# Kernel optimization log

Measured on AMD Instinct MI355X. Metric: run time of the kernel, lower is better.

## Reference

```python
import jax, jax.numpy as jnp
import numpy as np

DS = 16                      # downsample
DEPTH_MIN, DEPTH_MAX = 1.0, 60.0
XB = (-51.2, 51.2, 0.4)      # bev_x_bound
YB = (-51.2, 51.2, 0.4)      # bev_y_bound
ZB = (-5.0, 3.0)             # bev_z_bound (min, max)
BEV_H = int((YB[1] - YB[0]) / YB[2])   # 256
BEV_W = int((XB[1] - XB[0]) / XB[2])   # 256


def setup_inputs() -> dict:
    key = jax.random.key(0)
    k1, k2 = jax.random.split(key)
    B, N, C, H, W, D = 2, 6, 128, 16, 44, 64
    feat = jax.random.normal(k1, (B, N, C, H, W), dtype=jnp.float32)
    # depth distribution: softmax over depth bins (as a real LSS depth head produces)
    depth = jax.nn.softmax(jax.random.normal(k2, (B, N, D, H, W), dtype=jnp.float32), axis=2)
    # intrinsics chosen so that after the module's internal K scaling the frustum
    # rays actually spread over the BEV grid (non-degenerate valid mask)
    K = np.array([[2.0, 0.0, 1.34], [0.0, 2.0, 0.47], [0.0, 0.0, 1.0]], dtype=np.float32)
    intrinsics = np.broadcast_to(K, (B, N, 3, 3)).copy()
    # 6 cameras looking outward: cam(x right, y down, z fwd) -> ego(x fwd, y left, z up), yawed
    base = np.array([[0, 0, 1], [-1, 0, 0], [0, -1, 0]], dtype=np.float32)
    Es = []
    for yaw in np.linspace(0.0, 2.0 * np.pi, N, endpoint=False):
        c, s = np.cos(yaw), np.sin(yaw)
        Rz = np.array([[c, -s, 0], [s, c, 0], [0, 0, 1]], dtype=np.float32)
        E = np.eye(4, dtype=np.float32)
        E[:3, :3] = Rz @ base
        E[:3, 3] = [1.0 * c, 1.0 * s, 1.5]
        Es.append(E)
    extrinsics = np.broadcast_to(np.stack(Es), (B, N, 4, 4)).copy()
    return {
        "feat": feat,
        "depth": depth,
        "intrinsics": jnp.asarray(intrinsics),
        "extrinsics": jnp.asarray(extrinsics),
        "img_h": 256,
        "img_w": 704,
    }


def _forward(feat, depth, intrinsics, extrinsics, img_h, img_w):
    B, N, C, H, W = feat.shape
    D = depth.shape[2]
    dt = feat.dtype
    # frustum (D,H,W) of pixel coords u,v and metric depth d
    dbins = jnp.linspace(DEPTH_MIN, DEPTH_MAX, D).astype(dt)
    yy, xx = jnp.meshgrid(jnp.arange(H, dtype=dt), jnp.arange(W, dtype=dt), indexing='ij')
    u = jnp.broadcast_to(xx[None], (D, H, W)).reshape(-1)
    v = jnp.broadcast_to(yy[None], (D, H, W)).reshape(-1)
    d = jnp.broadcast_to(dbins[:, None, None], (D, H, W)).reshape(-1)
    # intrinsics scaled exactly as the torch module does (rows 0,1 scaled)
    scale_x = W / (img_w / DS)
    scale_y = H / (img_h / DS)
    rs = jnp.array([DS / scale_x, DS / scale_y, 1.0], dtype=dt)
    K = intrinsics * rs[:, None]            # (B,N,3,3)
    Kinv = jnp.linalg.inv(K)
    uvd = jnp.stack([u * d, v * d, d], axis=-1)     # (P,3), P = D*H*W
    pc = jnp.einsum('bnij,pj->bnpi', Kinv, uvd)     # camera-frame points
    R = extrinsics[..., :3, :3]
    t = extrinsics[..., :3, 3]
    pts = jnp.einsum('bnij,bnpj->bnpi', R, pc) + t[:, :, None, :]   # (B,N,P,3) ego
    pts = pts.reshape(B, -1, 3)                     # (B, N*P, 3)
    # depth-lift: feat (B,N,C,H,W) x depth (B,N,D,H,W) -> (B, N*D*H*W, C)
    lifted = (feat[:, :, :, None] * depth[:, :, None]).transpose(0, 1, 3, 4, 5, 2).reshape(B, -1, C)
    # voxelize (torch .long() truncates toward zero; so does astype here)
    xi = ((pts[..., 0] - XB[0]) / XB[2]).astype(jnp.int32)
    yi = ((pts[..., 1] - YB[0]) / YB[2]).astype(jnp.int32)
    valid = (xi >= 0) & (xi < BEV_W) & (yi >= 0) & (yi < BEV_H) & \
            (pts[..., 2] >= ZB[0]) & (pts[..., 2] <= ZB[1])
    idx = jnp.where(valid, yi * BEV_W + xi, 0)      # invalid -> cell 0 with zeroed value
    vals = lifted * valid[..., None].astype(dt)
    seg = lambda val, i: jax.ops.segment_sum(val, i, num_segments=BEV_H * BEV_W)
    bev = jax.vmap(seg)(vals, idx)                  # (B, cells, C)
    cnt = jax.vmap(seg)(valid.astype(dt), idx)      # (B, cells)
    bev = bev.transpose(0, 2, 1).reshape(B, C, BEV_H, BEV_W)
    cnt = cnt.reshape(B, 1, BEV_H, BEV_W)
    return bev / (cnt + 1e-5)


def reference(feat, depth, intrinsics, extrinsics, img_h, img_w):
    return _forward(feat, depth, intrinsics, extrinsics, img_h, img_w)
```

## Files before the change

kernel.cpp:

```cpp
#include <hip/hip_runtime.h>
#include <hip/hip_bf16.h>

#define Bc 2
#define Nc 6
#define Cc 128
#define Hc 16
#define Wc 44
#define Dc 64
#define HWc (Hc*Wc)
#define BNc (Bc*Nc)
#define NRAY (Nc*HWc)
#define NPTS (Bc*Nc*Dc*HWc)
#define BEV_W 256
#define BEV_H 256
#define BEV_HW (BEV_W*BEV_H)
#define NSEG (Bc*BEV_HW)
#define GT 16
#define NTILE (NSEG/GT)
#define NSCANB 512
#define GNB 1056
#define GNW (GNB*4)

#define OFF_KI    0
#define OFF_DB    512
#define OFF_CNT   1024
#define OFF_OFFS  (OFF_CNT  + 524288)
#define OFF_FILL  (OFF_OFFS + 524288)
#define OFF_BSUM  (OFF_FILL + 524288)
#define OFF_E8    (OFF_BSUM + 4096)
#define OFF_FT    (OFF_E8   + 4325376)
#define WS_NEED   (OFF_FT   + 4325376)
#define OFF_ACC   (OFF_FT   + 4325376)
#define WS_BIG    (OFF_ACC  + 67108864)
#define OFF_FIDX  OFF_E8
#define OFF_FCNT  OFF_CNT

__device__ __forceinline__ void setup_into(int tid, const float* __restrict__ intr,
                                           const int* __restrict__ p_imgh,
                                           const int* __restrict__ p_imgw,
                                           float* Ki, float* db) {
    if (tid < Dc) {
        double v = 1.0 + (double)tid * (59.0 / 63.0);
        db[tid] = (tid == Dc - 1) ? 60.0f : (float)v;
    }
    if (tid >= BNc) return;
    double img_h = (double)p_imgh[0];
    double img_w = (double)p_imgw[0];
    double scale_x = (double)Wc / (img_w / 16.0);
    double scale_y = (double)Hc / (img_h / 16.0);
    float rs0 = (float)(16.0 / scale_x);
    float rs1 = (float)(16.0 / scale_y);
    float rs2 = 1.0f;
    const float* K = intr + tid * 9;
    float k0 = __fmul_rn(K[0], rs0), k1 = __fmul_rn(K[1], rs0), k2 = __fmul_rn(K[2], rs0);
    float k3 = __fmul_rn(K[3], rs1), k4 = __fmul_rn(K[4], rs1), k5 = __fmul_rn(K[5], rs1);
    float k6 = __fmul_rn(K[6], rs2), k7 = __fmul_rn(K[7], rs2), k8 = __fmul_rn(K[8], rs2);
    float c0 = __fsub_rn(__fmul_rn(k4,k8), __fmul_rn(k5,k7));
    float c1 = __fsub_rn(__fmul_rn(k3,k8), __fmul_rn(k5,k6));
    float c2 = __fsub_rn(__fmul_rn(k3,k7), __fmul_rn(k4,k6));
    float det = __fadd_rn(__fsub_rn(__fmul_rn(k0,c0), __fmul_rn(k1,c1)), __fmul_rn(k2,c2));
    float* o = Ki + tid * 9;
    o[0] = __fdiv_rn(c0, det);
    o[1] = __fdiv_rn(__fsub_rn(__fmul_rn(k2,k7), __fmul_rn(k1,k8)), det);
    o[2] = __fdiv_rn(__fsub_rn(__fmul_rn(k1,k5), __fmul_rn(k2,k4)), det);
    o[3] = __fdiv_rn(__fsub_rn(__fmul_rn(k5,k6), __fmul_rn(k3,k8)), det);
    o[4] = __fdiv_rn(__fsub_rn(__fmul_rn(k0,k8), __fmul_rn(k2,k6)), det);
    o[5] = __fdiv_rn(__fsub_rn(__fmul_rn(k2,k3), __fmul_rn(k0,k5)), det);
    o[6] = __fdiv_rn(c2, det);
    o[7] = __fdiv_rn(__fsub_rn(__fmul_rn(k1,k6), __fmul_rn(k0,k7)), det);
    o[8] = __fdiv_rn(__fsub_rn(__fmul_rn(k0,k4), __fmul_rn(k1,k3)), det);
}

__global__ void k_setup(const float* __restrict__ intr, const float* __restrict__ extr,
                        const int* __restrict__ p_imgh, const int* __restrict__ p_imgw,
                        float* __restrict__ Ki, float* __restrict__ db) {
    setup_into(threadIdx.x, intr, p_imgh, p_imgw, Ki, db);
}

__device__ __forceinline__ int classify_point(int gid, const float* Ki_all,
                                              const float* db, const float* extr) {
    int p   = gid % HWc;
    int tmp = gid / HWc;
    int d   = tmp % Dc;
    int bn  = tmp / Dc;
    int w = p % Wc, h = p / Wc;
    float dd = db[d];
    float ud = __fmul_rn((float)w, dd);
    float vd = __fmul_rn((float)h, dd);
    const float* Ki = Ki_all + bn * 9;
    float pcx = fmaf(Ki[2], dd, fmaf(Ki[1], vd, __fmul_rn(Ki[0], ud)));
    float pcy = fmaf(Ki[5], dd, fmaf(Ki[4], vd, __fmul_rn(Ki[3], ud)));
    float pcz = fmaf(Ki[8], dd, fmaf(Ki[7], vd, __fmul_rn(Ki[6], ud)));
    const float* E = extr + bn * 16;
    float px = __fadd_rn(fmaf(E[2],  pcz, fmaf(E[1], pcy, __fmul_rn(E[0], pcx))), E[3]);
    float py = __fadd_rn(fmaf(E[6],  pcz, fmaf(E[5], pcy, __fmul_rn(E[4], pcx))), E[7]);
    float pz = __fadd_rn(fmaf(E[10], pcz, fmaf(E[9], pcy, __fmul_rn(E[8], pcx))), E[11]);
    float fx = __fdiv_rn(__fsub_rn(px, -51.2f), 0.4f);
    float fy = __fdiv_rn(__fsub_rn(py, -51.2f), 0.4f);
    int xi = (int)fx;
    int yi = (int)fy;
    bool valid = (xi >= 0) && (xi < BEV_W) && (yi >= 0) && (yi < BEV_H)
              && (pz >= -5.0f) && (pz <= 3.0f);
    return valid ? (yi * BEV_W + xi) : -1;
}

__device__ __forceinline__ void scan_bsum(int tid, const int* __restrict__ bsum,
                                          int* sB, int* su, int* pEtotS) {
    int2 v2 = ((const int2*)bsum)[tid];
    int s = v2.x + v2.y;
    su[tid] = s;
    __syncthreads();
    for (int st = 1; st < 256; st <<= 1) {
        int t2 = (tid >= st) ? su[tid - st] : 0;
        __syncthreads();
        su[tid] += t2;
        __syncthreads();
    }
    int base = su[tid] - s;
    sB[2 * tid]     = base;
    sB[2 * tid + 1] = base + v2.x;
    if (tid == 255) *pEtotS = base + s;
    __syncthreads();
}

__device__ __forceinline__ unsigned long long lanemask_le(int lane) {
    return (lane == 63) ? ~0ull : ((1ull << (lane + 1)) - 1ull);
}

__global__ __launch_bounds__(256) void k_count(const float* __restrict__ intr,
                                               const float* __restrict__ extr,
                                               const int* __restrict__ p_imgh,
                                               const int* __restrict__ p_imgw,
                                               const float* __restrict__ feat,
                                               int* __restrict__ cntArr,
                                               float* __restrict__ ft) {
    __shared__ float sKi[BNc * 9];
    __shared__ float sDb[Dc];
    __shared__ float buf[Cc * 17];
    int tid = threadIdx.x;
    setup_into(tid, intr, p_imgh, p_imgw, sKi, sDb);
    __syncthreads();
    int gid = blockIdx.x * 256 + tid;
    int cell = classify_point(gid, sKi, sDb, extr);
    {
        int lane = tid & 63;
        int b = gid / (Nc * Dc * HWc);
        int seg = b * BEV_HW + cell;
        int key = (cell >= 0) ? seg : -1;
        int pk  = __shfl_up(key, 1);
        bool bnd = (lane == 0) || (key != pk);
        unsigned long long bm = __ballot(bnd);
        if (key >= 0 && bnd) {
            unsigned long long rest = (lane == 63) ? 0ull : (bm >> (lane + 1));
            int runlen = (rest != 0ull) ? __ffsll((long long)rest) : (64 - lane);
            atomicAdd(&cntArr[seg], runlen);
        }
    }
    if (blockIdx.x < BNc * (HWc / 16)) {
        int bn   = blockIdx.x / (HWc / 16);
        int tile = blockIdx.x % (HWc / 16);
        const float* fb = feat + (size_t)bn * Cc * HWc + tile * 16;
        for (int i = tid; i < Cc * 16; i += 256) {
            int c = i >> 4, hw = i & 15;
            buf[c * 17 + hw] = fb[c * HWc + hw];
        }
        __syncthreads();
        float* obt = ft + ((size_t)bn * HWc + tile * 16) * Cc;
        for (int i = tid; i < 16 * Cc; i += 256) {
            int r = i >> 7, ch = i & 127;
            obt[(size_t)r * Cc + ch] = buf[ch * 17 + r];
        }
    }
}

__global__ __launch_bounds__(256) void k_scanB(const int* __restrict__ cntArr,
                                               int* __restrict__ offs,
                                               int* __restrict__ fill,
                                               int* __restrict__ bsum) {
    __shared__ int su[256];
    int tid = threadIdx.x;
    int g = blockIdx.x * 256 + tid;
    int v = cntArr[g];
    su[tid] = v;
    __syncthreads();
    for (int st = 1; st < 256; st <<= 1) {
        int t2 = (tid >= st) ? su[tid - st] : 0;
        __syncthreads();
        su[tid] += t2;
        __syncthreads();
    }
    int e = su[tid] - v;
    offs[g] = e;
    fill[g] = e;
    if (tid == 255) bsum[blockIdx.x] = su[255];
}

__global__ __launch_bounds__(256) void k_fill(const float* __restrict__ intr,
                                              const float* __restrict__ extr,
                                              const int* __restrict__ p_imgh,
                                              const int* __restrict__ p_imgw,
                                              const float* __restrict__ depth,
                                              int* __restrict__ fill,
                                              const int* __restrict__ bsum,
                                              int2* __restrict__ e8) {
    __shared__ float sKi[BNc * 9];
    __shared__ float sDb[Dc];
    __shared__ int   sB[NSCANB];
    __shared__ int   su[256];
    __shared__ int   sEtot;
    int tid = threadIdx.x;
    setup_into(tid, intr, p_imgh, p_imgw, sKi, sDb);
    scan_bsum(tid, bsum, sB, su, &sEtot);
    int gid = blockIdx.x * 256 + tid;
    int cell = classify_point(gid, sKi, sDb, extr);
    int lane = tid & 63;
    int bnum = gid / (Nc * Dc * HWc);
    int seg = bnum * BEV_HW + cell;
    int key = (cell >= 0) ? seg : -1;
    int pk  = __shfl_up(key, 1);
    bool bnd = (lane == 0) || (key != pk);
    unsigned long long bm = __ballot(bnd);
    int base = 0;
    if (key >= 0 && bnd) {
        unsigned long long rest = (lane == 63) ? 0ull : (bm >> (lane + 1));
        int runlen = (rest != 0ull) ? __ffsll((long long)rest) : (64 - lane);
        base = atomicAdd(&fill[seg], runlen) + sB[seg >> 8];
    }
    int headLane = 63 - __clzll(bm & lanemask_le(lane));
    int myBase = __shfl(base, headLane);
    if (key >= 0) {
        int p   = gid % HWc;
        int bn  = gid / (Dc * HWc);
        int ray = (bn % Nc) * HWc + p;
        e8[myBase + (lane - headLane)] = make_int2(ray | (seg << 13),
                                                   __float_as_int(depth[gid]));
    }
}

__global__ __launch_bounds__(256) void k_gather2(const float2* __restrict__ ft2,
                                                 const int2* __restrict__ e8,
                                                 const int* __restrict__ cntArr,
                                                 const int* __restrict__ offs,
                                                 const int* __restrict__ bsum,
                                                 float* __restrict__ acc) {
    __shared__ int sB[NSCANB];
    __shared__ int su[256];
    __shared__ int sEtot;
    int tid = threadIdx.x;
    scan_bsum(tid, bsum, sB, su, &sEtot);
    int Etot = sEtot;
    int wid  = blockIdx.x * 4 + (tid >> 6);
    int lane = tid & 63;
    int WCH  = (Etot + GNW - 1) / GNW;
    if (WCH <= 0) return;
    int start = wid * WCH;
    if (start >= Etot) return;
    int end = start + WCH; if (end > Etot) end = Etot;
    int k0 = 0;
    if (start > 0) {
        int segP = e8[start - 1].x >> 13;
        k0 = offs[segP] + sB[segP >> 8] + cntArr[segP];
        if (k0 >= end) return;
    }
    int segE = e8[end - 1].x >> 13;
    int kend = offs[segE] + sB[segE >> 8] + cntArr[segE];
    int total = kend - k0;

    float2 a = make_float2(0.f, 0.f);
    int curc = -1;
    const int U = 8;
    int nb = total / U;
    if (nb > 0) {
        int2 e[U];
        #pragma unroll
        for (int u = 0; u < U; u++) e[u] = e8[k0 + u];
        for (int g = 0; g < nb; g++) {
            float2 f[U];
            #pragma unroll
            for (int u = 0; u < U; u++) {
                int sx = e[u].x;
                f[u] = ft2[((size_t)((sx >> 29) * NRAY) + (sx & 8191)) * 64 + lane];
            }
            int2 en[U];
            if (g + 1 < nb) {
                #pragma unroll
                for (int u = 0; u < U; u++) en[u] = e8[k0 + (g + 1) * U + u];
            } else {
                #pragma unroll
                for (int u = 0; u < U; u++) en[u] = e[u];
            }
            #pragma unroll
            for (int u = 0; u < U; u++) {
                int sg = e[u].x >> 13;
                if (sg != curc) {
                    if (curc >= 0) *(float2*)(acc + (size_t)curc * Cc + 2 * lane) = a;
                    curc = sg; a.x = 0.f; a.y = 0.f;
                }
                float ww = __int_as_float(e[u].y);
                a.x = fmaf(ww, f[u].x, a.x);
                a.y = fmaf(ww, f[u].y, a.y);
            }
            #pragma unroll
            for (int u = 0; u < U; u++) e[u] = en[u];
        }
    }
    for (int j = nb * U; j < total; j++) {
        int2 ee = e8[k0 + j];
        int sg = ee.x >> 13;
        if (sg != curc) {
            if (curc >= 0) *(float2*)(acc + (size_t)curc * Cc + 2 * lane) = a;
            curc = sg; a.x = 0.f; a.y = 0.f;
        }
        float ww = __int_as_float(ee.y);
        float2 f = ft2[((size_t)((ee.x >> 29) * NRAY) + (ee.x & 8191)) * 64 + lane];
        a.x = fmaf(ww, f.x, a.x);
        a.y = fmaf(ww, f.y, a.y);
    }
    if (curc >= 0) *(float2*)(acc + (size_t)curc * Cc + 2 * lane) = a;
}

__global__ __launch_bounds__(256) void k_finish(const float* __restrict__ acc,
                                                const int* __restrict__ cntArr,
                                                float* __restrict__ out) {
    __shared__ float res[GT * 132];
    __shared__ float sInv[GT];
    __shared__ int   sC[GT + 1];
    int seg0  = blockIdx.x * GT;
    int b     = seg0 >> 16;
    int cell0 = seg0 & 65535;
    int tid = threadIdx.x;
    if (tid < 64) {
        int n = (tid < GT) ? cntArr[seg0 + tid] : 0;
        int v = n;
        #pragma unroll
        for (int d = 1; d < GT; d <<= 1) {
            int y = __shfl_up(v, d, GT);
            if ((tid & (GT - 1)) >= d) v += y;
        }
        if (tid < GT) {
            sC[tid] = n;
            sInv[tid] = __fdiv_rn(1.0f, __fadd_rn((float)n, 1e-5f));
            if (tid == GT - 1) sC[GT] = v;
        }
    }
    __syncthreads();
    float* ob = out + (size_t)b * Cc * BEV_HW + cell0;
    if (sC[GT] == 0) {
        float4 z = {0.f, 0.f, 0.f, 0.f};
        for (int i = tid; i < Cc * GT / 4; i += 256) {
            int q = i & 3, c = i >> 2;
            *(float4*)(ob + (size_t)c * BEV_HW + q * 4) = z;
        }
        return;
    }
    {
        int g0 = tid >> 5, l32 = tid & 31;
        #pragma unroll
        for (int pass = 0; pass < 2; pass++) {
            int g = g0 + pass * 8;
            float4 v;
            if (sC[g] > 0) v = *(const float4*)(acc + (size_t)(seg0 + g) * Cc + 4 * l32);
            else           v = make_float4(0.f, 0.f, 0.f, 0.f);
            *(float4*)(&res[g * 132 + 4 * l32]) = v;
        }
    }
    __syncthreads();
    for (int i = tid; i < Cc * GT / 4; i += 256) {
        int q = i & 3, c = i >> 2;
        float4 v;
        #pragma unroll
        for (int kk = 0; kk < 4; kk++) {
            int g = q * 4 + kk;
            (&v.x)[kk] = __fmul_rn(res[g * 132 + c], sInv[g]);
        }
        *(float4*)(ob + (size_t)c * BEV_HW + q * 4) = v;
    }
}

__global__ __launch_bounds__(256) void k_classifyF(const float* __restrict__ Ki_all,
                                                   const float* __restrict__ db,
                                                   const float* __restrict__ extr,
                                                   int* __restrict__ idxT,
                                                   float* __restrict__ cnt) {
    int gid = blockIdx.x * 256 + threadIdx.x;
    if (gid >= NPTS) return;
    int cell = classify_point(gid, Ki_all, db, extr);
    idxT[gid] = cell;
    if (cell >= 0) {
        int b = gid / (Nc * Dc * HWc);
        atomicAdd(&cnt[b * BEV_HW + cell], 1.0f);
    }
}

__global__ __launch_bounds__(256) void k_scatterF(const float* __restrict__ feat,
                                                  const float* __restrict__ depth,
                                                  const int* __restrict__ idxT,
                                                  float* __restrict__ out) {
    __shared__ float s_dw[HWc];
    __shared__ int   s_idx[HWc];
    int blk = blockIdx.x;
    int bn  = blk / Dc;
    int b   = bn / Nc;
    int tid = threadIdx.x;
    const float* dp = depth + (size_t)blk * HWc;
    const int*   ip = idxT  + (size_t)blk * HWc;
    for (int p = tid; p < HWc; p += 256) { s_dw[p] = dp[p]; s_idx[p] = ip[p]; }
    __syncthreads();
    const float* fb = feat + (size_t)bn * Cc * HWc;
    float*       ob = out  + (size_t)b  * Cc * BEV_HW;
    for (int c = 0; c < Cc; c++) {
        const float* f = fb + (size_t)c * HWc;
        float*       o = ob + (size_t)c * BEV_HW;
        for (int p = tid; p < HWc; p += 256) {
            int cell = s_idx[p];
            if (cell >= 0) atomicAdd(&o[cell], __fmul_rn(f[p], s_dw[p]));
        }
    }
}

__global__ __launch_bounds__(256) void k_normF(float* __restrict__ out,
                                               const float* __restrict__ cnt) {
    int i = blockIdx.x * 256 + threadIdx.x;
    const int total = Bc * Cc * BEV_HW / 4;
    if (i >= total) return;
    int q = i % (BEV_HW / 4);
    int b = i / (Cc * BEV_HW / 4);
    float4 v = ((float4*)out)[i];
    float4 cv = ((const float4*)cnt)[b * (BEV_HW / 4) + q];
    v.x = __fdiv_rn(v.x, __fadd_rn(cv.x, 1e-5f));
    v.y = __fdiv_rn(v.y, __fadd_rn(cv.y, 1e-5f));
    v.z = __fdiv_rn(v.z, __fadd_rn(cv.z, 1e-5f));
    v.w = __fdiv_rn(v.w, __fadd_rn(cv.w, 1e-5f));
    ((float4*)out)[i] = v;
}

extern "C" void kernel_launch(void* const* d_in, const int* in_sizes, int n_in,
                              void* d_out, int out_size, void* d_ws, size_t ws_size,
                              hipStream_t stream) {
    const float* feat  = (const float*)d_in[0];
    const float* depth = (const float*)d_in[1];
    const float* intr  = (const float*)d_in[2];
    const float* extr  = (const float*)d_in[3];
    const int*   imh   = (const int*)d_in[4];
    const int*   imw   = (const int*)d_in[5];
    float* out = (float*)d_out;
    char*  ws  = (char*)d_ws;

    if (ws_size >= (size_t)WS_BIG) {
        int*   cntA = (int*)(ws + OFF_CNT);
        int*   offs = (int*)(ws + OFF_OFFS);
        int*   fill = (int*)(ws + OFF_FILL);
        int*   bsum = (int*)(ws + OFF_BSUM);
        int2*  e8   = (int2*)(ws + OFF_E8);
        float* ft   = (float*)(ws + OFF_FT);
        float* acc  = (float*)(ws + OFF_ACC);

        hipMemsetAsync(cntA, 0, (size_t)NSEG * sizeof(int), stream);
        k_count<<<NPTS / 256, 256, 0, stream>>>(intr, extr, imh, imw, feat, cntA, ft);
        k_scanB<<<NSCANB, 256, 0, stream>>>(cntA, offs, fill, bsum);
        k_fill<<<NPTS / 256, 256, 0, stream>>>(intr, extr, imh, imw, depth, fill, bsum, e8);
        k_gather2<<<GNB, 256, 0, stream>>>((const float2*)ft, e8, cntA, offs, bsum, acc);
        k_finish<<<NTILE, 256, 0, stream>>>(acc, cntA, out);
    } else {
        float* Ki   = (float*)(ws + OFF_KI);
        float* db   = (float*)(ws + OFF_DB);
        int*   idxT = (int*)(ws + OFF_FIDX);
        float* cnt  = (float*)(ws + OFF_FCNT);
        hipMemsetAsync(out, 0, (size_t)out_size * sizeof(float), stream);
        hipMemsetAsync(cnt, 0, (size_t)Bc * BEV_HW * sizeof(float), stream);
        k_setup<<<1, 64, 0, stream>>>(intr, extr, imh, imw, Ki, db);
        k_classifyF<<<(NPTS + 255) / 256, 256, 0, stream>>>(Ki, db, extr, idxT, cnt);
        k_scatterF<<<Bc * Nc * Dc, 256, 0, stream>>>(feat, depth, idxT, out);
        k_normF<<<(Bc * Cc * BEV_HW / 4 + 255) / 256, 256, 0, stream>>>(out, cnt);
    }
}
```

Before: 152.1 us.

## Fuse normalization into gather, precompute ranks in count pass, drop finish kernel

The count kernel now records each point's segment and its rank within that segment. The fill kernel then becomes a simple scatter, with no second classification and no atomics, using a fully scanned offsets array produced by a new small scan kernel. The gather kernel stages per-warp accumulators for 16-cell groups in shared memory and writes normalized output directly. Extra blocks zero the empty cells. This removes the 64MB accumulator round trip and the finish kernel. In exchange, output writes are strided and less coalesced, and there is an extra pk buffer pass.

```diff
diff --git a/kernel.cpp b/kernel.cpp
--- a/kernel.cpp
+++ b/kernel.cpp
@@ -15,11 +15,12 @@
 #define BEV_H 256
 #define BEV_HW (BEV_W*BEV_H)
 #define NSEG (Bc*BEV_HW)
-#define GT 16
-#define NTILE (NSEG/GT)
 #define NSCANB 512
-#define GNB 1056
+#define NGRP (NSEG/16)
+#define GNB 768
 #define GNW (GNB*4)
+#define ZNB 256
+#define ZNW (ZNB*4)
 
 #define OFF_KI    0
 #define OFF_DB    512
@@ -27,6 +28,7 @@
 #define OFF_OFFS  (OFF_CNT  + 524288)
 #define OFF_FILL  (OFF_OFFS + 524288)
 #define OFF_BSUM  (OFF_FILL + 524288)
+#define OFF_ETOT  (OFF_BSUM + 2048)
 #define OFF_E8    (OFF_BSUM + 4096)
 #define OFF_FT    (OFF_E8   + 4325376)
 #define WS_NEED   (OFF_FT   + 4325376)
@@ -133,6 +135,7 @@
                                                const int* __restrict__ p_imgw,
                                                const float* __restrict__ feat,
                                                int* __restrict__ cntArr,
+                                               unsigned* __restrict__ pk,
                                                float* __restrict__ ft) {
     __shared__ float sKi[BNc * 9];
     __shared__ float sDb[Dc];
@@ -147,14 +150,20 @@
         int b = gid / (Nc * Dc * HWc);
         int seg = b * BEV_HW + cell;
         int key = (cell >= 0) ? seg : -1;
-        int pk  = __shfl_up(key, 1);
-        bool bnd = (lane == 0) || (key != pk);
+        int pkey = __shfl_up(key, 1);
+        bool bnd = (lane == 0) || (key != pkey);
         unsigned long long bm = __ballot(bnd);
+        int base = 0;
         if (key >= 0 && bnd) {
             unsigned long long rest = (lane == 63) ? 0ull : (bm >> (lane + 1));
             int runlen = (rest != 0ull) ? __ffsll((long long)rest) : (64 - lane);
-            atomicAdd(&cntArr[seg], runlen);
-        }
+            base = atomicAdd(&cntArr[seg], runlen);
+        }
+        int headLane = 63 - __clzll(bm & lanemask_le(lane));
+        int rbase = __shfl(base, headLane);
+        pk[gid] = (key >= 0)
+                ? ((unsigned)seg | ((unsigned)(rbase + (lane - headLane)) << 17))
+                : 0xFFFFFFFFu;
     }
     if (blockIdx.x < BNc * (HWc / 16)) {
         int bn   = blockIdx.x / (HWc / 16);
@@ -175,7 +184,6 @@
 
 __global__ __launch_bounds__(256) void k_scanB(const int* __restrict__ cntArr,
                                                int* __restrict__ offs,
-                                               int* __restrict__ fill,
                                                int* __restrict__ bsum) {
     __shared__ int su[256];
     int tid = threadIdx.x;
@@ -189,68 +197,110 @@
         su[tid] += t2;
         __syncthreads();
     }
-    int e = su[tid] - v;
-    offs[g] = e;
-    fill[g] = e;
+    offs[g] = su[tid] - v;
     if (tid == 255) bsum[blockIdx.x] = su[255];
 }
 
-__global__ __launch_bounds__(256) void k_fill(const float* __restrict__ intr,
-                                              const float* __restrict__ extr,
-                                              const int* __restrict__ p_imgh,
-                                              const int* __restrict__ p_imgw,
+__global__ __launch_bounds__(256) void k_scanT(int* __restrict__ offs,
+                                               const int* __restrict__ bsum,
+                                               int* __restrict__ EtotG) {
+    __shared__ int sB[NSCANB];
+    __shared__ int su[256];
+    __shared__ int sE;
+    int tid = threadIdx.x;
+    scan_bsum(tid, bsum, sB, su, &sE);
+    int add = sB[blockIdx.x];
+    int g = blockIdx.x * 256 + tid;
+    offs[g] += add;
+    if (blockIdx.x == 0 && tid == 0) *EtotG = sE;
+}
+
+__global__ __launch_bounds__(256) void k_fill(const unsigned* __restrict__ pk,
                                               const float* __restrict__ depth,
-                                              int* __restrict__ fill,
-                                              const int* __restrict__ bsum,
+                                              const int* __restrict__ offs,
                                               int2* __restrict__ e8) {
-    __shared__ float sKi[BNc * 9];
-    __shared__ float sDb[Dc];
-    __shared__ int   sB[NSCANB];
-    __shared__ int   su[256];
-    __shared__ int   sEtot;
-    int tid = threadIdx.x;
-    setup_into(tid, intr, p_imgh, p_imgw, sKi, sDb);
-    scan_bsum(tid, bsum, sB, su, &sEtot);
-    int gid = blockIdx.x * 256 + tid;
-    int cell = classify_point(gid, sKi, sDb, extr);
-    int lane = tid & 63;
-    int bnum = gid / (Nc * Dc * HWc);
-    int seg = bnum * BEV_HW + cell;
-    int key = (cell >= 0) ? seg : -1;
-    int pk  = __shfl_up(key, 1);
-    bool bnd = (lane == 0) || (key != pk);
-    unsigned long long bm = __ballot(bnd);
-    int base = 0;
-    if (key >= 0 && bnd) {
-        unsigned long long rest = (lane == 63) ? 0ull : (bm >> (lane + 1));
-        int runlen = (rest != 0ull) ? __ffsll((long long)rest) : (64 - lane);
-        base = atomicAdd(&fill[seg], runlen) + sB[seg >> 8];
-    }
-    int headLane = 63 - __clzll(bm & lanemask_le(lane));
-    int myBase = __shfl(base, headLane);
-    if (key >= 0) {
-        int p   = gid % HWc;
-        int bn  = gid / (Dc * HWc);
-        int ray = (bn % Nc) * HWc + p;
-        e8[myBase + (lane - headLane)] = make_int2(ray | (seg << 13),
-                                                   __float_as_int(depth[gid]));
-    }
-}
-
-__global__ __launch_bounds__(256) void k_gather2(const float2* __restrict__ ft2,
+    int gid = blockIdx.x * 256 + threadIdx.x;
+    unsigned v = pk[gid];
+    if (v == 0xFFFFFFFFu) return;
+    int seg  = (int)(v & (unsigned)(NSEG - 1));
+    int rank = (int)(v >> 17);
+    int pos  = offs[seg] + rank;
+    int p  = gid % HWc;
+    int bn = gid / (Dc * HWc);
+    int ray = (bn % Nc) * HWc + p;
+    e8[pos] = make_int2(ray | (seg << 13), __float_as_int(depth[gid]));
+}
+
+__device__ __noinline__ void flush_group(const float* winw, const float* sNw,
+                                         float* __restrict__ out,
+                                         unsigned mask, int g16, int lane) {
+    asm volatile("s_waitcnt lgkmcnt(0)" ::: "memory");
+    int b = g16 >> 12;
+    int cell0 = (g16 & 4095) << 4;
+    float* ob = out + (size_t)b * Cc * BEV_HW + cell0;
+    int g = lane & 15, cq = lane >> 4;
+    bool own = (mask >> g) & 1u;
+    float inv = __fdiv_rn(1.0f, __fadd_rn(sNw[g], 1e-5f));
+    #pragma unroll 4
+    for (int c4 = 0; c4 < Cc; c4 += 4) {
+        int c = c4 + cq;
+        if (own) ob[(size_t)c * BEV_HW + g] = __fmul_rn(winw[g * 132 + c], inv);
+    }
+}
+
+#define GF_STEP(EE, FF) do {                                                    \
+    int sg_ = (EE).x >> 13;                                                     \
+    if (sg_ != curc) {                                                          \
+        if (curc >= 0) {                                                        \
+            *(float2*)&winw[(curc & 15) * 132 + 2 * lane] = a;                  \
+            if (lane == 0) sNw[curc & 15] = (float)segN;                        \
+            mask |= 1u << (curc & 15);                                          \
+            if ((sg_ >> 4) != (curc >> 4)) {                                    \
+                flush_group(winw, sNw, out, mask, curc >> 4, lane);             \
+                mask = 0;                                                       \
+            }                                                                   \
+        }                                                                       \
+        curc = sg_; a.x = 0.f; a.y = 0.f; segN = 0;                             \
+    }                                                                           \
+    segN++;                                                                     \
+    float ww_ = __int_as_float((EE).y);                                         \
+    a.x = fmaf(ww_, (FF).x, a.x);                                               \
+    a.y = fmaf(ww_, (FF).y, a.y);                                               \
+} while (0)
+
+__global__ __launch_bounds__(256) void k_gatherF(const float2* __restrict__ ft2,
                                                  const int2* __restrict__ e8,
                                                  const int* __restrict__ cntArr,
                                                  const int* __restrict__ offs,
-                                                 const int* __restrict__ bsum,
-                                                 float* __restrict__ acc) {
-    __shared__ int sB[NSCANB];
-    __shared__ int su[256];
-    __shared__ int sEtot;
+                                                 const int* __restrict__ EtotG,
+                                                 float* __restrict__ out) {
+    __shared__ float win[4][16 * 132];
+    __shared__ float sN[4][16];
     int tid = threadIdx.x;
-    scan_bsum(tid, bsum, sB, su, &sEtot);
-    int Etot = sEtot;
-    int wid  = blockIdx.x * 4 + (tid >> 6);
-    int lane = tid & 63;
+    int w = tid >> 6, lane = tid & 63;
+
+    if (blockIdx.x >= GNB) {
+        int zwid = (blockIdx.x - GNB) * 4 + w;
+        int g = lane & 15, cq = lane >> 4;
+        for (int g16 = zwid; g16 < NGRP; g16 += ZNW) {
+            int n = (lane < 16) ? cntArr[(g16 << 4) + lane] : 1;
+            unsigned long long bz = __ballot(n == 0);
+            unsigned em = (unsigned)bz & 0xFFFFu;
+            if (em == 0) continue;
+            int b = g16 >> 12;
+            int cell0 = (g16 & 4095) << 4;
+            float* ob = out + (size_t)b * Cc * BEV_HW + cell0;
+            bool own = (em >> g) & 1u;
+            #pragma unroll 4
+            for (int c4 = 0; c4 < Cc; c4 += 4) {
+                if (own) ob[(size_t)(c4 + cq) * BEV_HW + g] = 0.f;
+            }
+        }
+        return;
+    }
+
+    int Etot = *EtotG;
+    int wid  = blockIdx.x * 4 + w;
     int WCH  = (Etot + GNW - 1) / GNW;
     if (WCH <= 0) return;
     int start = wid * WCH;
@@ -259,22 +309,27 @@
     int k0 = 0;
     if (start > 0) {
         int segP = e8[start - 1].x >> 13;
-        k0 = offs[segP] + sB[segP >> 8] + cntArr[segP];
+        k0 = offs[segP] + cntArr[segP];
         if (k0 >= end) return;
     }
     int segE = e8[end - 1].x >> 13;
-    int kend = offs[segE] + sB[segE >> 8] + cntArr[segE];
+    int kend = offs[segE] + cntArr[segE];
     int total = kend - k0;
 
+    float* winw = win[w];
+    float* sNw  = sN[w];
     float2 a = make_float2(0.f, 0.f);
     int curc = -1;
+    int segN = 0;
+    unsigned mask = 0;
+
     const int U = 8;
     int nb = total / U;
     if (nb > 0) {
         int2 e[U];
         #pragma unroll
         for (int u = 0; u < U; u++) e[u] = e8[k0 + u];
-        for (int g = 0; g < nb; g++) {
+        for (int gI = 0; gI < nb; gI++) {
             float2 f[U];
             #pragma unroll
             for (int u = 0; u < U; u++) {
@@ -282,98 +337,30 @@
                 f[u] = ft2[((size_t)((sx >> 29) * NRAY) + (sx & 8191)) * 64 + lane];
             }
             int2 en[U];
-            if (g + 1 < nb) {
+            if (gI + 1 < nb) {
                 #pragma unroll
-                for (int u = 0; u < U; u++) en[u] = e8[k0 + (g + 1) * U + u];
+                for (int u = 0; u < U; u++) en[u] = e8[k0 + (gI + 1) * U + u];
             } else {
                 #pragma unroll
                 for (int u = 0; u < U; u++) en[u] = e[u];
             }
             #pragma unroll
-            for (int u = 0; u < U; u++) {
-                int sg = e[u].x >> 13;
-                if (sg != curc) {
-                    if (curc >= 0) *(float2*)(acc + (size_t)curc * Cc + 2 * lane) = a;
-                    curc = sg; a.x = 0.f; a.y = 0.f;
-                }
-                float ww = __int_as_float(e[u].y);
-                a.x = fmaf(ww, f[u].x, a.x);
-                a.y = fmaf(ww, f[u].y, a.y);
-            }
+            for (int u = 0; u < U; u++) GF_STEP(e[u], f[u]);
             #pragma unroll
             for (int u = 0; u < U; u++) e[u] = en[u];
         }
     }
     for (int j = nb * U; j < total; j++) {
         int2 ee = e8[k0 + j];
-        int sg = ee.x >> 13;
-        if (sg != curc) {
-            if (curc >= 0) *(float2*)(acc + (size_t)curc * Cc + 2 * lane) = a;
-            curc = sg; a.x = 0.f; a.y = 0.f;
-        }
-        float ww = __int_as_float(ee.y);
-        float2 f = ft2[((size_t)((ee.x >> 29) * NRAY) + (ee.x & 8191)) * 64 + lane];
-        a.x = fmaf(ww, f.x, a.x);
-        a.y = fmaf(ww, f.y, a.y);
-    }
-    if (curc >= 0) *(float2*)(acc + (size_t)curc * Cc + 2 * lane) = a;
-}
-
-__global__ __launch_bounds__(256) void k_finish(const float* __restrict__ acc,
-                                                const int* __restrict__ cntArr,
-                                                float* __restrict__ out) {
-    __shared__ float res[GT * 132];
-    __shared__ float sInv[GT];
-    __shared__ int   sC[GT + 1];
-    int seg0  = blockIdx.x * GT;
-    int b     = seg0 >> 16;
-    int cell0 = seg0 & 65535;
-    int tid = threadIdx.x;
-    if (tid < 64) {
-        int n = (tid < GT) ? cntArr[seg0 + tid] : 0;
-        int v = n;
-        #pragma unroll
-        for (int d = 1; d < GT; d <<= 1) {
-            int y = __shfl_up(v, d, GT);
-            if ((tid & (GT - 1)) >= d) v += y;
-        }
-        if (tid < GT) {
-            sC[tid] = n;
-            sInv[tid] = __fdiv_rn(1.0f, __fadd_rn((float)n, 1e-5f));
-            if (tid == GT - 1) sC[GT] = v;
-        }
-    }
-    __syncthreads();
-    float* ob = out + (size_t)b * Cc * BEV_HW + cell0;
-    if (sC[GT] == 0) {
-        float4 z = {0.f, 0.f, 0.f, 0.f};
-        for (int i = tid; i < Cc * GT / 4; i += 256) {
-            int q = i & 3, c = i >> 2;
-            *(float4*)(ob + (size_t)c * BEV_HW + q * 4) = z;
-        }
-        return;
-    }
-    {
-        int g0 = tid >> 5, l32 = tid & 31;
-        #pragma unroll
-        for (int pass = 0; pass < 2; pass++) {
-            int g = g0 + pass * 8;
-            float4 v;
-            if (sC[g] > 0) v = *(const float4*)(acc + (size_t)(seg0 + g) * Cc + 4 * l32);
-            else           v = make_float4(0.f, 0.f, 0.f, 0.f);
-            *(float4*)(&res[g * 132 + 4 * l32]) = v;
-        }
-    }
-    __syncthreads();
-    for (int i = tid; i < Cc * GT / 4; i += 256) {
-        int q = i & 3, c = i >> 2;
-        float4 v;
-        #pragma unroll
-        for (int kk = 0; kk < 4; kk++) {
-            int g = q * 4 + kk;
-            (&v.x)[kk] = __fmul_rn(res[g * 132 + c], sInv[g]);
-        }
-        *(float4*)(ob + (size_t)c * BEV_HW + q * 4) = v;
+        int sx = ee.x;
+        float2 f = ft2[((size_t)((sx >> 29) * NRAY) + (sx & 8191)) * 64 + lane];
+        GF_STEP(ee, f);
+    }
+    if (curc >= 0) {
+        *(float2*)&winw[(curc & 15) * 132 + 2 * lane] = a;
+        if (lane == 0) sNw[curc & 15] = (float)segN;
+        mask |= 1u << (curc & 15);
+        flush_group(winw, sNw, out, mask, curc >> 4, lane);
     }
 }
 
@@ -447,20 +434,20 @@
     char*  ws  = (char*)d_ws;
 
     if (ws_size >= (size_t)WS_BIG) {
-        int*   cntA = (int*)(ws + OFF_CNT);
-        int*   offs = (int*)(ws + OFF_OFFS);
-        int*   fill = (int*)(ws + OFF_FILL);
-        int*   bsum = (int*)(ws + OFF_BSUM);
-        int2*  e8   = (int2*)(ws + OFF_E8);
-        float* ft   = (float*)(ws + OFF_FT);
-        float* acc  = (float*)(ws + OFF_ACC);
+        int*      cntA  = (int*)(ws + OFF_CNT);
+        int*      offs  = (int*)(ws + OFF_OFFS);
+        int*      bsum  = (int*)(ws + OFF_BSUM);
+        int*      EtotG = (int*)(ws + OFF_ETOT);
+        int2*     e8    = (int2*)(ws + OFF_E8);
+        float*    ft    = (float*)(ws + OFF_FT);
+        unsigned* pk    = (unsigned*)(ws + OFF_ACC);
 
         hipMemsetAsync(cntA, 0, (size_t)NSEG * sizeof(int), stream);
-        k_count<<<NPTS / 256, 256, 0, stream>>>(intr, extr, imh, imw, feat, cntA, ft);
-        k_scanB<<<NSCANB, 256, 0, stream>>>(cntA, offs, fill, bsum);
-        k_fill<<<NPTS / 256, 256, 0, stream>>>(intr, extr, imh, imw, depth, fill, bsum, e8);
-        k_gather2<<<GNB, 256, 0, stream>>>((const float2*)ft, e8, cntA, offs, bsum, acc);
-        k_finish<<<NTILE, 256, 0, stream>>>(acc, cntA, out);
+        k_count<<<NPTS / 256, 256, 0, stream>>>(intr, extr, imh, imw, feat, cntA, pk, ft);
+        k_scanB<<<NSCANB, 256, 0, stream>>>(cntA, offs, bsum);
+        k_scanT<<<NSCANB, 256, 0, stream>>>(offs, bsum, EtotG);
+        k_fill<<<NPTS / 256, 256, 0, stream>>>(pk, depth, offs, e8);
+        k_gatherF<<<GNB + ZNB, 256, 0, stream>>>((const float2*)ft, e8, cntA, offs, EtotG, out);
     } else {
         float* Ki   = (float*)(ws + OFF_KI);
         float* db   = (float*)(ws + OFF_DB);
```

Result: slower. 163.6 us (+7.5%).
